# Kernel tuning notes

Hardware: AMD Instinct MI355X
Metric: run time of the kernel (lower is better)

Reference implementation:

```python
import jax, jax.numpy as jnp
import numpy as np

EMB = 512
HEADS = 8
B, T = 8, 1024

def setup_inputs() -> dict:
    key = jax.random.key(0)
    ks = jax.random.split(key, 6)
    e, h = EMB, HEADS
    s = 1.0 / np.sqrt(e)
    x = jax.random.normal(ks[0], (B, T, e), dtype=jnp.float32)
    # Linear(emb, emb*heads, bias=False): stored as (e, e*h) for x @ W
    Wk = jax.random.normal(ks[1], (e, e * h), dtype=jnp.float32) * s
    Wq = jax.random.normal(ks[2], (e, e * h), dtype=jnp.float32) * s
    Wv = jax.random.normal(ks[3], (e, e * h), dtype=jnp.float32) * s
    # unifyheads: Linear(heads*emb, emb) with bias
    Wu = jax.random.normal(ks[4], (e * h, e), dtype=jnp.float32) * (1.0 / np.sqrt(e * h))
    bu = jax.random.normal(ks[5], (e,), dtype=jnp.float32) * 0.01
    return {"x": x, "Wk": Wk, "Wq": Wq, "Wv": Wv, "Wu": Wu, "bu": bu}

def reference(x, Wk, Wq, Wv, Wu, bu):
    b, t, e = x.shape
    h = HEADS
    scale = e ** (-0.25)  # applied to both q and k, as in the torch code
    q = (x @ Wq).reshape(b, t, h, e) * scale  # (b,t,h,e)
    k = (x @ Wk).reshape(b, t, h, e) * scale
    v = (x @ Wv).reshape(b, t, h, e)
    dot = jnp.einsum('bqhe,bkhe->bhqk', q, k)      # (b,h,t,t)
    attn = jax.nn.softmax(dot, axis=-1)
    out = jnp.einsum('bhqk,bkhe->bqhe', attn, v)    # (b,t,h,e)
    out = out.reshape(b, t, h * e)
    return out @ Wu + bu                            # (b,t,e)
```

## Files before the change

### kernel.cpp

```cpp
#include <hip/hip_runtime.h>
#include <hip/hip_bf16.h>
#include <cstdint>

typedef __attribute__((ext_vector_type(8))) short bf16x8;
typedef __attribute__((ext_vector_type(4))) float f32x4;

typedef __attribute__((address_space(1))) const void gv_t;
typedef __attribute__((address_space(3))) void lv_t;

__device__ __forceinline__ unsigned short f2b(float f) {
  __hip_bfloat16 h = __float2bfloat16(f);
  return __builtin_bit_cast(unsigned short, h);
}
__device__ __forceinline__ float b2f(unsigned short u) {
  unsigned int x = (unsigned int)u << 16;
  return __builtin_bit_cast(float, x);
}

__global__ __launch_bounds__(256) void k_cast(const float* __restrict__ src,
                                              unsigned short* __restrict__ dst, int n4) {
  int i = blockIdx.x * 256 + threadIdx.x;
  if (i >= n4) return;
  const float4 v = ((const float4*)src)[i];
  ushort4 o;
  o.x = f2b(v.x); o.y = f2b(v.y); o.z = f2b(v.z); o.w = f2b(v.w);
  ((ushort4*)dst)[i] = o;
}

__global__ void k_transpose_cast(const float* __restrict__ src,
                                 unsigned short* __restrict__ dst, int R, int C) {
  __shared__ float tile[32][33];
  const int tx = threadIdx.x, ty = threadIdx.y;
  const int c0 = blockIdx.x * 32, r0 = blockIdx.y * 32;
#pragma unroll
  for (int i = 0; i < 32; i += 8)
    tile[ty + i][tx] = src[(long)(r0 + ty + i) * C + (c0 + tx)];
  __syncthreads();
#pragma unroll
  for (int i = 0; i < 32; i += 8)
    dst[(long)(c0 + ty + i) * R + (r0 + tx)] = f2b(tile[tx][ty + i]);
}

__global__ void k_transpose_cast3(const float* __restrict__ s0, const float* __restrict__ s1,
                                  const float* __restrict__ s2,
                                  unsigned short* __restrict__ dst, int R, int C) {
  const float* src = (blockIdx.z == 0) ? s0 : ((blockIdx.z == 1) ? s1 : s2);
  unsigned short* d = dst + (size_t)blockIdx.z * R * C;
  __shared__ float tile[32][33];
  const int tx = threadIdx.x, ty = threadIdx.y;
  const int c0 = blockIdx.x * 32, r0 = blockIdx.y * 32;
#pragma unroll
  for (int i = 0; i < 32; i += 8)
    tile[ty + i][tx] = src[(long)(r0 + ty + i) * C + (c0 + tx)];
  __syncthreads();
#pragma unroll
  for (int i = 0; i < 32; i += 8)
    d[(long)(c0 + ty + i) * R + (r0 + tx)] = f2b(tile[tx][ty + i]);
}

enum { EPI_QK = 0, EPI_VT = 1 };

#define BAR256() do { asm volatile("" ::: "memory"); __builtin_amdgcn_s_barrier(); asm volatile("" ::: "memory"); } while (0)
#define WAITVM(n) do { asm volatile("s_waitcnt vmcnt(" #n ")" ::: "memory"); __builtin_amdgcn_sched_barrier(0); } while (0)

#define STAGE_A(tt, hw, qq)                                                                     \
  __builtin_amdgcn_global_load_lds(                                                            \
    (gv_t*)(A + (long)(m0 + (hw)*128 + (qq)*64 + rr) * lda + ((tt) << 6) + csw),               \
    (lv_t*)(&L[(((((tt)&1)*2 + (hw))*128 + (qq)*64 + rr))*64 + c0]), 16, 0, 0)

#define STAGE_B(tt, qi)                                                                         \
  __builtin_amdgcn_global_load_lds(                                                            \
    (gv_t*)(Bt + (long)(n0 + (qi)*64 + rr) * ldb + ((tt) << 6) + csw),                         \
    (lv_t*)(&L[32768 + (((((tt)&1)*2 + ((qi)>>1))*128 + ((qi)&1)*64 + rr))*64 + c0]), 16, 0, 0)

#define PHASE(slot, QR, QC) do {                                                                \
    const unsigned short* Abase = &L[((slot)*2 + wr) * 8192];                                   \
    const unsigned short* Bbase = &L[32768 + ((slot)*2 + (wc>>1)) * 8192];                      \
    bf16x8 afr[4][2], bfr[2][2];                                                                \
    _Pragma("unroll")                                                                           \
    for (int fr = 0; fr < 4; ++fr) {                                                            \
      const int rA = (QR)*64 + fr*16 + l15;                                                     \
      _Pragma("unroll")                                                                         \
      for (int kk = 0; kk < 2; ++kk) {                                                          \
        const int cA = (kk*32 + l4*8) ^ ((rA & 7) << 3);                                        \
        afr[fr][kk] = *(const bf16x8*)(Abase + rA*64 + cA);                                     \
      }                                                                                         \
    }                                                                                           \
    _Pragma("unroll")                                                                           \
    for (int fc = 0; fc < 2; ++fc) {                                                            \
      const int rB = (wc&1)*64 + (QC)*32 + fc*16 + l15;                                         \
      _Pragma("unroll")                                                                         \
      for (int kk = 0; kk < 2; ++kk) {                                                          \
        const int cB = (kk*32 + l4*8) ^ ((rB & 7) << 3);                                        \
        bfr[fc][kk] = *(const bf16x8*)(Bbase + rB*64 + cB);                                     \
      }                                                                                         \
    }                                                                                           \
    __builtin_amdgcn_s_setprio(1);                                                              \
    _Pragma("unroll")                                                                           \
    for (int fr = 0; fr < 4; ++fr)                                                              \
      _Pragma("unroll")                                                                         \
      for (int fc = 0; fc < 2; ++fc)                                                            \
        _Pragma("unroll")                                                                       \
        for (int kk = 0; kk < 2; ++kk)                                                          \
          acc[(QR)*4+fr][(QC)*2+fc] = __builtin_amdgcn_mfma_f32_16x16x32_bf16(                  \
              afr[fr][kk], bfr[fc][kk], acc[(QR)*4+fr][(QC)*2+fc], 0, 0, 0);                    \
    __builtin_amdgcn_s_setprio(0);                                                              \
  } while (0)

template <int EPI>
__global__ __launch_bounds__(512)
void k_gemm256(const unsigned short* __restrict__ A, const unsigned short* __restrict__ Bt,
               void* __restrict__ Cv, int K, int lda, int ldb, float scale) {
  const int m0 = blockIdx.y * 256;
  const int n0 = blockIdx.x * 256;
  __shared__ __align__(16) unsigned short L[65536];
  const int tid = threadIdx.x;
  const int lane = tid & 63;
  const int wid = tid >> 6;
  const int wr = wid >> 2;
  const int wc = wid & 3;
  const int l15 = lane & 15;
  const int l4 = lane >> 4;
  const int rr = tid >> 3;
  const int c0 = (tid & 7) * 8;
  const int csw = c0 ^ ((rr & 7) << 3);

  f32x4 acc[8][4] = {};
  const int NT = K >> 6;

  STAGE_A(0, 0, 0); STAGE_A(0, 1, 0); STAGE_A(0, 0, 1); STAGE_A(0, 1, 1);
  STAGE_B(0, 0); STAGE_B(0, 1); STAGE_B(0, 2); STAGE_B(0, 3);
  if (NT > 1) {
    STAGE_A(1, 0, 0); STAGE_A(1, 1, 0);
    WAITVM(2);
  } else {
    WAITVM(0);
  }
  __builtin_amdgcn_s_barrier();
  asm volatile("" ::: "memory");

  for (int t = 0; t < NT; ++t) {
    const int slot = t & 1;
    if (t + 1 < NT) { STAGE_A(t + 1, 0, 1); STAGE_A(t + 1, 1, 1); }
    PHASE(slot, 0, 0);
    BAR256();
    if (t + 1 < NT) { STAGE_B(t + 1, 0); STAGE_B(t + 1, 1); }
    PHASE(slot, 0, 1);
    BAR256();
    if (t + 1 < NT) { STAGE_B(t + 1, 2); STAGE_B(t + 1, 3); }
    if (t + 2 < NT) { STAGE_A(t + 2, 0, 0); STAGE_A(t + 2, 1, 0); }
    PHASE(slot, 1, 0);
    BAR256();
    PHASE(slot, 1, 1);
    if (t + 1 < NT) {
      if (t + 2 < NT) WAITVM(2);
      else            WAITVM(0);
      __builtin_amdgcn_s_barrier();
      asm volatile("" ::: "memory");
    }
  }

#pragma unroll
  for (int i = 0; i < 8; ++i) {
#pragma unroll
    for (int j = 0; j < 4; ++j) {
#pragma unroll
      for (int r = 0; r < 4; ++r) {
        const int row = m0 + wr * 128 + i * 16 + l4 * 4 + r;
        const int col = n0 + wc * 64 + j * 16 + l15;
        const float v = acc[i][j][r];
        if (EPI == EPI_QK) {
          unsigned short* o = (unsigned short*)Cv;
          const int sec = col >> 12;
          const int cc = col & 4095;
          const long addr = (long)sec * 33554432 +
              ((long)((row >> 10) * 8 + (cc >> 9)) * 1024 + (row & 1023)) * 512 + (cc & 511);
          o[addr] = f2b(v * scale);
        } else {
          unsigned short* o = (unsigned short*)Cv;
          const long addr = (long)((col >> 10) * 8 + (row >> 9)) * 524288 +
                            (long)(row & 511) * 1024 + (col & 1023);
          o[addr] = f2b(v);
        }
      }
    }
  }
}

#define VSWZ(e) ((((e) & 3) ^ (((e) >> 2) & 3)))
__global__ __launch_bounds__(512)
void k_attn(unsigned short* __restrict__ q,
            const unsigned short* __restrict__ k,
            const unsigned short* __restrict__ vt)
{
  __shared__ __align__(16) unsigned short Qs[64 * 512];
  __shared__ __align__(16) unsigned short Ks[32 * 512];
  __shared__ __align__(16) unsigned short Vs[512 * 32];
  __shared__ __align__(16) unsigned short Es[64 * 40];
  const int bid = blockIdx.x;
  const int head = (bid & 7) * 8 + ((bid >> 3) >> 4);
  const int qt = (bid >> 3) & 15;
  const int tid = threadIdx.x;
  const int w = tid >> 6, lane = tid & 63;
  const int l15 = lane & 15, l4 = lane >> 4;
  const int qf = w & 3, kf = w >> 2;

  unsigned short* qg = q + (size_t)(head * 1024 + qt * 64) * 512;
  const unsigned short* kg = k + (size_t)head * 524288;
  const unsigned short* vg = vt + (size_t)head * 524288;

#pragma unroll
  for (int i = 0; i < 8; ++i) {
    const int row = i * 8 + w;
    __builtin_amdgcn_global_load_lds((gv_t*)(qg + (size_t)row * 512 + 8 * (lane ^ (row & 7))),
                                     (lv_t*)(&Qs[row * 512 + lane * 8]), 16, 0, 0);
  }
#pragma unroll
  for (int i = 0; i < 4; ++i) {
    const int row = i * 8 + w;
    __builtin_amdgcn_global_load_lds((gv_t*)(kg + (size_t)row * 512 + 8 * (lane ^ (row & 7))),
                                     (lv_t*)(&Ks[row * 512 + lane * 8]), 16, 0, 0);
  }
  __syncthreads();

  f32x4 acc[4][4] = {};
  float partial = 0.f;
  const int erow = tid >> 3;
  const int ej = tid & 7;
  const int eidx = 40 * erow + ej * 4;
  const int qrow = qf * 16 + l15;
  const int krow = kf * 16 + l15;

  for (int c = 0; c < 32; ++c) {
#pragma unroll
    for (int i = 0; i < 4; ++i) {
      const int r0 = i * 128 + w * 16;
      const int e = r0 + (lane >> 2);
      __builtin_amdgcn_global_load_lds(
          (gv_t*)(vg + (size_t)e * 1024 + c * 32 + 8 * ((lane & 3) ^ VSWZ(e))),
          (lv_t*)(&Vs[r0 * 32 + lane * 8]), 16, 0, 0);
    }
    f32x4 sacc0 = {0.f, 0.f, 0.f, 0.f};
    f32x4 sacc1 = {0.f, 0.f, 0.f, 0.f};
#pragma unroll
    for (int ks = 0; ks < 16; ks += 2) {
      bf16x8 aq0 = *(const bf16x8*)(&Qs[qrow * 512 + 8 * ((ks * 4 + l4) ^ (qrow & 7))]);
      bf16x8 bk0 = *(const bf16x8*)(&Ks[krow * 512 + 8 * ((ks * 4 + l4) ^ (krow & 7))]);
      sacc0 = __builtin_amdgcn_mfma_f32_16x16x32_bf16(aq0, bk0, sacc0, 0, 0, 0);
      bf16x8 aq1 = *(const bf16x8*)(&Qs[qrow * 512 + 8 * (((ks + 1) * 4 + l4) ^ (qrow & 7))]);
      bf16x8 bk1 = *(const bf16x8*)(&Ks[krow * 512 + 8 * (((ks + 1) * 4 + l4) ^ (krow & 7))]);
      sacc1 = __builtin_amdgcn_mfma_f32_16x16x32_bf16(aq1, bk1, sacc1, 0, 0, 0);
    }
#pragma unroll
    for (int r = 0; r < 4; ++r) {
      const int qq = qf * 16 + l4 * 4 + r;
      const int kk2 = kf * 16 + l15;
      Es[40 * qq + kk2] = f2b(__expf(sacc0[r] + sacc1[r]));
    }
    __syncthreads();
    if (c + 1 < 32) {
#pragma unroll
      for (int i = 0; i < 4; ++i) {
        const int row = i * 8 + w;
        __builtin_amdgcn_global_load_lds(
            (gv_t*)(kg + (size_t)((c + 1) * 32 + row) * 512 + 8 * (lane ^ (row & 7))),
            (lv_t*)(&Ks[row * 512 + lane * 8]), 16, 0, 0);
      }
    }
    {
      const ushort4 ev = *(const ushort4*)(&Es[eidx]);
      partial += (b2f(ev.x) + b2f(ev.y)) + (b2f(ev.z) + b2f(ev.w));
    }
    bf16x8 bv[4];
#pragma unroll
    for (int cf = 0; cf < 4; ++cf) {
      const int e = w * 64 + cf * 16 + l15;
      bv[cf] = *(const bf16x8*)(&Vs[e * 32 + 8 * (l4 ^ VSWZ(e))]);
    }
#pragma unroll
    for (int qf2 = 0; qf2 < 4; ++qf2) {
      const int qq = qf2 * 16 + l15;
      bf16x8 ae = *(const bf16x8*)(&Es[40 * qq + 8 * l4]);
#pragma unroll
      for (int cf = 0; cf < 4; ++cf)
        acc[qf2][cf] = __builtin_amdgcn_mfma_f32_16x16x32_bf16(ae, bv[cf], acc[qf2][cf], 0, 0, 0);
    }
    __syncthreads();
  }

  float* fs = (float*)Ks;
  fs[tid] = partial;
  __syncthreads();
  if (tid < 64) {
    float s = 0.f;
#pragma unroll
    for (int j = 0; j < 8; ++j) s += fs[tid * 8 + j];
    fs[512 + tid] = 1.0f / s;
  }
  __syncthreads();

#pragma unroll
  for (int qf2 = 0; qf2 < 4; ++qf2) {
#pragma unroll
    for (int r = 0; r < 4; ++r) {
      const int qq = qf2 * 16 + l4 * 4 + r;
      const float iv = fs[512 + qq];
#pragma unroll
      for (int cf = 0; cf < 4; ++cf) {
        const int e = w * 64 + cf * 16 + l15;
        qg[(size_t)qq * 512 + e] = f2b(acc[qf2][cf][r] * iv);
      }
    }
  }
}

__global__ __launch_bounds__(256)
void k_gemm_out(const unsigned short* __restrict__ A, const unsigned short* __restrict__ Bt,
                float* __restrict__ C, const float* __restrict__ bias) {
  const int m0 = blockIdx.y * 128;
  const int n0 = blockIdx.x * 128;
  __shared__ __align__(16) unsigned short As[2][128 * 32];
  __shared__ __align__(16) unsigned short Bs[2][128 * 32];
  const int tid = threadIdx.x;
  const int lane = tid & 63;
  const int wm = ((tid >> 6) >> 1) * 64;
  const int wn = ((tid >> 6) & 1) * 64;
  const int srow = tid >> 2;
  const int scol = (tid & 3) * 8;
  f32x4 acc[4][4] = {};

  const int row1 = m0 + srow, row2 = row1 + 64;
  const size_t hb1 = (size_t)(row1 >> 10) * 8 * 524288 + (size_t)(row1 & 1023) * 512;
  const size_t hb2 = (size_t)(row2 >> 10) * 8 * 524288 + (size_t)(row2 & 1023) * 512;
  const unsigned short* gb = Bt + (size_t)(n0 + srow) * 4096 + scol;

#define STAGEO(buf, k0) do {                                                                          \
    const size_t koffA = (size_t)((k0) >> 9) * 524288 + ((k0) & 511) + scol;                          \
    __builtin_amdgcn_global_load_lds((gv_t*)(A + hb1 + koffA), (lv_t*)(&As[buf][tid * 8]), 16, 0, 0);  \
    __builtin_amdgcn_global_load_lds((gv_t*)(A + hb2 + koffA), (lv_t*)(&As[buf][tid * 8 + 2048]), 16, 0, 0); \
    __builtin_amdgcn_global_load_lds((gv_t*)(gb + (k0)), (lv_t*)(&Bs[buf][tid * 8]), 16, 0, 0);        \
    __builtin_amdgcn_global_load_lds((gv_t*)(gb + 64L * 4096 + (k0)), (lv_t*)(&Bs[buf][tid * 8 + 2048]), 16, 0, 0); \
  } while (0)

  STAGEO(0, 0);
  for (int k0 = 0; k0 < 4096; k0 += 32) {
    const int cur = (k0 >> 5) & 1;
    __syncthreads();
    if (k0 + 32 < 4096) { STAGEO(cur ^ 1, k0 + 32); }
    const unsigned short* ap = &As[cur][(wm + (lane & 15)) * 32 + (lane >> 4) * 8];
    const unsigned short* bp = &Bs[cur][(wn + (lane & 15)) * 32 + (lane >> 4) * 8];
    bf16x8 fa[4], fb[4];
#pragma unroll
    for (int i = 0; i < 4; ++i) fa[i] = *(const bf16x8*)(ap + i * 16 * 32);
#pragma unroll
    for (int i = 0; i < 4; ++i) fb[i] = *(const bf16x8*)(bp + i * 16 * 32);
#pragma unroll
    for (int mi = 0; mi < 4; ++mi)
#pragma unroll
      for (int ni = 0; ni < 4; ++ni)
        acc[mi][ni] = __builtin_amdgcn_mfma_f32_16x16x32_bf16(fa[mi], fb[ni], acc[mi][ni], 0, 0, 0);
  }
#undef STAGEO

#pragma unroll
  for (int mi = 0; mi < 4; ++mi) {
#pragma unroll
    for (int ni = 0; ni < 4; ++ni) {
#pragma unroll
      for (int r = 0; r < 4; ++r) {
        const int row = m0 + wm + mi * 16 + ((lane >> 4) * 4 + r);
        const int col = n0 + wn + ni * 16 + (lane & 15);
        C[(long)row * 512 + col] = acc[mi][ni][r] + bias[col];
      }
    }
  }
}

extern "C" void kernel_launch(void* const* d_in, const int* in_sizes, int n_in,
                              void* d_out, int out_size, void* d_ws, size_t ws_size,
                              hipStream_t stream) {
  const float* x  = (const float*)d_in[0];
  const float* Wk = (const float*)d_in[1];
  const float* Wq = (const float*)d_in[2];
  const float* Wv = (const float*)d_in[3];
  const float* Wu = (const float*)d_in[4];
  const float* bu = (const float*)d_in[5];
  float* out = (float*)d_out;
  char* ws = (char*)d_ws;

  const size_t NEED = 226492416;
  if (ws_size < NEED) return;

  unsigned short* wut   = (unsigned short*)(ws + 0);
  unsigned short* wtqkv = (unsigned short*)(ws + 4194304);
  unsigned short* xb    = (unsigned short*)(ws + 16777216);
  unsigned short* qb    = (unsigned short*)(ws + 25165824);
  unsigned short* kb    = qb + 33554432;
  unsigned short* vtb   = qb + 67108864;

  const float s4 = 0.21022410381342865f;

  k_cast<<<4096, 256, 0, stream>>>(x, xb, 1048576);
  k_transpose_cast3<<<dim3(128, 16, 3), dim3(32, 8), 0, stream>>>(Wq, Wk, Wv, wtqkv, 512, 4096);
  k_transpose_cast<<<dim3(16, 128), dim3(32, 8), 0, stream>>>(Wu, wut, 4096, 512);

  k_gemm256<EPI_QK><<<dim3(32, 32, 1), 512, 0, stream>>>(xb, wtqkv, qb, 512, 512, 512, s4);
  k_gemm256<EPI_VT><<<dim3(32, 16, 1), 512, 0, stream>>>(wtqkv + 4194304, xb, vtb, 512, 512, 512, 1.0f);

  k_attn<<<1024, 512, 0, stream>>>(qb, kb, vtb);

  k_gemm_out<<<dim3(4, 64, 1), 256, 0, stream>>>(qb, wut, out, bu);
}
```

Before: 500.6 us.

## Double-buffer K/V/E tiles in attention and hold Q fragments in registers

The attention kernel now keeps its Q fragments in registers, loaded directly from global memory, instead of staging Q in LDS. K, V and the exp tile are double-buffered in LDS so the next chunk's V and the chunk after next's K load asynchronously during compute. Explicit vmcnt/lgkmcnt waits with raw barriers replace the __syncthreads calls, and s_setprio raises priority around the MFMA loops. This hides global-load latency and frees LDS, at the cost of more registers (16 bf16x8 Q fragments) that could reduce occupancy, plus fragile hand-counted waits.

```diff
diff --git a/kernel.cpp b/kernel.cpp
--- a/kernel.cpp
+++ b/kernel.cpp
@@ -62,6 +62,7 @@
 
 #define BAR256() do { asm volatile("" ::: "memory"); __builtin_amdgcn_s_barrier(); asm volatile("" ::: "memory"); } while (0)
 #define WAITVM(n) do { asm volatile("s_waitcnt vmcnt(" #n ")" ::: "memory"); __builtin_amdgcn_sched_barrier(0); } while (0)
+#define WAITLG() do { asm volatile("s_waitcnt lgkmcnt(0)" ::: "memory"); } while (0)
 
 #define STAGE_A(tt, hw, qq)                                                                     \
   __builtin_amdgcn_global_load_lds(                                                            \
@@ -188,15 +189,37 @@
 }
 
 #define VSWZ(e) ((((e) & 3) ^ (((e) >> 2) & 3)))
+
+__device__ __forceinline__ void stage_k(const unsigned short* kg, unsigned short* dst,
+                                        int c, int w, int lane) {
+#pragma unroll
+  for (int i = 0; i < 4; ++i) {
+    const int row = i * 8 + w;
+    __builtin_amdgcn_global_load_lds(
+        (gv_t*)(kg + (size_t)(c * 32 + row) * 512 + 8 * (lane ^ (row & 7))),
+        (lv_t*)(dst + row * 512 + lane * 8), 16, 0, 0);
+  }
+}
+__device__ __forceinline__ void stage_v(const unsigned short* vg, unsigned short* dst,
+                                        int c, int w, int lane) {
+#pragma unroll
+  for (int i = 0; i < 4; ++i) {
+    const int r0 = i * 128 + w * 16;
+    const int e = r0 + (lane >> 2);
+    __builtin_amdgcn_global_load_lds(
+        (gv_t*)(vg + (size_t)e * 1024 + c * 32 + 8 * ((lane & 3) ^ VSWZ(e))),
+        (lv_t*)(dst + r0 * 32 + lane * 8), 16, 0, 0);
+  }
+}
+
 __global__ __launch_bounds__(512)
 void k_attn(unsigned short* __restrict__ q,
             const unsigned short* __restrict__ k,
             const unsigned short* __restrict__ vt)
 {
-  __shared__ __align__(16) unsigned short Qs[64 * 512];
-  __shared__ __align__(16) unsigned short Ks[32 * 512];
-  __shared__ __align__(16) unsigned short Vs[512 * 32];
-  __shared__ __align__(16) unsigned short Es[64 * 40];
+  __shared__ __align__(16) unsigned short Ks[2][16384];
+  __shared__ __align__(16) unsigned short Vs[2][16384];
+  __shared__ __align__(16) unsigned short Es[2][2560];
   const int bid = blockIdx.x;
   const int head = (bid & 7) * 8 + ((bid >> 3) >> 4);
   const int qt = (bid >> 3) & 15;
@@ -209,86 +232,78 @@
   const unsigned short* kg = k + (size_t)head * 524288;
   const unsigned short* vg = vt + (size_t)head * 524288;
 
-#pragma unroll
-  for (int i = 0; i < 8; ++i) {
-    const int row = i * 8 + w;
-    __builtin_amdgcn_global_load_lds((gv_t*)(qg + (size_t)row * 512 + 8 * (lane ^ (row & 7))),
-                                     (lv_t*)(&Qs[row * 512 + lane * 8]), 16, 0, 0);
-  }
-#pragma unroll
-  for (int i = 0; i < 4; ++i) {
-    const int row = i * 8 + w;
-    __builtin_amdgcn_global_load_lds((gv_t*)(kg + (size_t)row * 512 + 8 * (lane ^ (row & 7))),
-                                     (lv_t*)(&Ks[row * 512 + lane * 8]), 16, 0, 0);
-  }
-  __syncthreads();
+  const int qrow = qf * 16 + l15;
+  const int krow = kf * 16 + l15;
+
+  bf16x8 q_r[16];
+#pragma unroll
+  for (int ks = 0; ks < 16; ++ks)
+    q_r[ks] = *(const bf16x8*)(qg + (size_t)qrow * 512 + (size_t)(ks * 4 + l4) * 8);
+
+  stage_k(kg, &Ks[0][0], 0, w, lane);
+  stage_v(vg, &Vs[0][0], 0, w, lane);
+  stage_k(kg, &Ks[1][0], 1, w, lane);
 
   f32x4 acc[4][4] = {};
   float partial = 0.f;
   const int erow = tid >> 3;
   const int ej = tid & 7;
   const int eidx = 40 * erow + ej * 4;
-  const int qrow = qf * 16 + l15;
-  const int krow = kf * 16 + l15;
 
   for (int c = 0; c < 32; ++c) {
-#pragma unroll
-    for (int i = 0; i < 4; ++i) {
-      const int r0 = i * 128 + w * 16;
-      const int e = r0 + (lane >> 2);
-      __builtin_amdgcn_global_load_lds(
-          (gv_t*)(vg + (size_t)e * 1024 + c * 32 + 8 * ((lane & 3) ^ VSWZ(e))),
-          (lv_t*)(&Vs[r0 * 32 + lane * 8]), 16, 0, 0);
-    }
+    unsigned short* KsC = &Ks[c & 1][0];
+    unsigned short* VsC = &Vs[c & 1][0];
+    unsigned short* EsC = &Es[c & 1][0];
+    if (c < 31) { WAITVM(4); } else { WAITVM(0); }
+    WAITLG();
+    __builtin_amdgcn_s_barrier();
+    asm volatile("" ::: "memory");
+    if (c + 1 < 32) stage_v(vg, &Vs[(c + 1) & 1][0], c + 1, w, lane);
     f32x4 sacc0 = {0.f, 0.f, 0.f, 0.f};
     f32x4 sacc1 = {0.f, 0.f, 0.f, 0.f};
+    __builtin_amdgcn_s_setprio(1);
 #pragma unroll
     for (int ks = 0; ks < 16; ks += 2) {
-      bf16x8 aq0 = *(const bf16x8*)(&Qs[qrow * 512 + 8 * ((ks * 4 + l4) ^ (qrow & 7))]);
-      bf16x8 bk0 = *(const bf16x8*)(&Ks[krow * 512 + 8 * ((ks * 4 + l4) ^ (krow & 7))]);
-      sacc0 = __builtin_amdgcn_mfma_f32_16x16x32_bf16(aq0, bk0, sacc0, 0, 0, 0);
-      bf16x8 aq1 = *(const bf16x8*)(&Qs[qrow * 512 + 8 * (((ks + 1) * 4 + l4) ^ (qrow & 7))]);
-      bf16x8 bk1 = *(const bf16x8*)(&Ks[krow * 512 + 8 * (((ks + 1) * 4 + l4) ^ (krow & 7))]);
-      sacc1 = __builtin_amdgcn_mfma_f32_16x16x32_bf16(aq1, bk1, sacc1, 0, 0, 0);
-    }
+      bf16x8 bk0 = *(const bf16x8*)(&KsC[krow * 512 + 8 * ((ks * 4 + l4) ^ (krow & 7))]);
+      sacc0 = __builtin_amdgcn_mfma_f32_16x16x32_bf16(q_r[ks], bk0, sacc0, 0, 0, 0);
+      bf16x8 bk1 = *(const bf16x8*)(&KsC[krow * 512 + 8 * (((ks + 1) * 4 + l4) ^ (krow & 7))]);
+      sacc1 = __builtin_amdgcn_mfma_f32_16x16x32_bf16(q_r[ks + 1], bk1, sacc1, 0, 0, 0);
+    }
+    __builtin_amdgcn_s_setprio(0);
 #pragma unroll
     for (int r = 0; r < 4; ++r) {
       const int qq = qf * 16 + l4 * 4 + r;
       const int kk2 = kf * 16 + l15;
-      Es[40 * qq + kk2] = f2b(__expf(sacc0[r] + sacc1[r]));
-    }
-    __syncthreads();
-    if (c + 1 < 32) {
-#pragma unroll
-      for (int i = 0; i < 4; ++i) {
-        const int row = i * 8 + w;
-        __builtin_amdgcn_global_load_lds(
-            (gv_t*)(kg + (size_t)((c + 1) * 32 + row) * 512 + 8 * (lane ^ (row & 7))),
-            (lv_t*)(&Ks[row * 512 + lane * 8]), 16, 0, 0);
-      }
-    }
+      EsC[40 * qq + kk2] = f2b(__expf(sacc0[r] + sacc1[r]));
+    }
+    WAITLG();
+    __builtin_amdgcn_s_barrier();
+    asm volatile("" ::: "memory");
+    if (c + 2 < 32) stage_k(kg, KsC, c + 2, w, lane);
     {
-      const ushort4 ev = *(const ushort4*)(&Es[eidx]);
+      const ushort4 ev = *(const ushort4*)(&EsC[eidx]);
       partial += (b2f(ev.x) + b2f(ev.y)) + (b2f(ev.z) + b2f(ev.w));
     }
     bf16x8 bv[4];
 #pragma unroll
     for (int cf = 0; cf < 4; ++cf) {
       const int e = w * 64 + cf * 16 + l15;
-      bv[cf] = *(const bf16x8*)(&Vs[e * 32 + 8 * (l4 ^ VSWZ(e))]);
-    }
+      bv[cf] = *(const bf16x8*)(&VsC[e * 32 + 8 * (l4 ^ VSWZ(e))]);
+    }
+    __builtin_amdgcn_s_setprio(1);
 #pragma unroll
     for (int qf2 = 0; qf2 < 4; ++qf2) {
       const int qq = qf2 * 16 + l15;
-      bf16x8 ae = *(const bf16x8*)(&Es[40 * qq + 8 * l4]);
+      bf16x8 ae = *(const bf16x8*)(&EsC[40 * qq + 8 * l4]);
 #pragma unroll
       for (int cf = 0; cf < 4; ++cf)
         acc[qf2][cf] = __builtin_amdgcn_mfma_f32_16x16x32_bf16(ae, bv[cf], acc[qf2][cf], 0, 0, 0);
     }
-    __syncthreads();
-  }
-
-  float* fs = (float*)Ks;
+    __builtin_amdgcn_s_setprio(0);
+  }
+
+  __syncthreads();
+  float* fs = (float*)&Ks[0][0];
   fs[tid] = partial;
   __syncthreads();
   if (tid < 64) {
```

Result: faster. 470.4 us (-6.0%).
